# Kernel tuning notes

Measured on AMD Instinct MI355X. Metric: run time of the kernel, lower is better.

The kernel has to match this reference:

```python
import jax, jax.numpy as jnp
import numpy as np

N_NODES = 100000
N_EDGES = 6400000
MIN_DIST = 5.0


def setup_inputs() -> dict:
    key = jax.random.key(0)
    k1, k2, k3 = jax.random.split(key, 3)
    pos = jax.random.normal(k1, (N_NODES, 2), dtype=jnp.float32)
    vel = jax.random.normal(k2, (N_NODES, 2), dtype=jnp.float32)
    edge_index = jax.random.randint(k3, (2, N_EDGES), 0, N_NODES, dtype=jnp.int64)
    return {"pos": pos, "vel": vel, "edge_index": edge_index}


def reference(pos, vel, edge_index):
    # h = [pos, vel] per node, shape [N, 4]
    h = jnp.concatenate([pos, vel], axis=-1)
    src, dst = edge_index[0], edge_index[1]  # PyG: h_j = h[src], h_i = h[dst]
    h_dif = h[src] - h[dst]                  # [E, 4]
    pos_dif = h_dif[:, :2]                   # [E, 2]
    vel_dif = h_dif[:, 2:]                   # [E, 2]

    norm = jnp.linalg.norm(pos_dif, axis=1)  # [E]
    safe_norm = jnp.where(norm > 0, norm, 1.0)
    # coll = -sigmoid(-10*(|d|-min_dist)) * d/|d|, nan_to_num(0) where |d|==0
    coll = jnp.where(
        (norm > 0)[:, None],
        -jax.nn.sigmoid(-10.0 * (norm - MIN_DIST))[:, None] * pos_dif / safe_norm[:, None],
        0.0,
    )                                        # [E, 2]
    mean_in = pos_dif / 30.0 + vel_dif       # [E, 2]

    n = pos.shape[0]
    add_out = jax.ops.segment_sum(coll, dst, num_segments=n)      # scatter add
    sums = jax.ops.segment_sum(mean_in, dst, num_segments=n)
    counts = jax.ops.segment_sum(jnp.ones((dst.shape[0], 1), pos.dtype), dst, num_segments=n)
    mean_out = sums / jnp.maximum(counts, 1.0)                    # scatter mean

    return add_out * 5.0 + mean_out          # [N, 2] acceleration
```

## Files before the change

### kernel.cpp

```cpp
#include <hip/hip_runtime.h>


#define DC      200
#define NBK     512
#define NSEG    512
#define EPB     12500
#define ORDCAP  14400
#define KB      13
#define KBV     16
#define KMAX    15
#define BLOCK   256
#define BBLOCK  1024
#define FBLOCK  1024

__device__ __forceinline__ void edge_math(float4 hs, float4 hd,
                                          float& cx, float& cy, float& mx, float& my) {
    float px = hs.x - hd.x;
    float py = hs.y - hd.y;
    float vx = hs.z - hd.z;
    float vy = hs.w - hd.w;
    float norm = sqrtf(px * px + py * py);
    cx = 0.0f; cy = 0.0f;
    if (norm > 0.0f) {
        float sig = 1.0f / (1.0f + expf(10.0f * (norm - 5.0f)));
        float scale = -sig / norm;
        cx = scale * px;
        cy = scale * py;
    }
    mx = px * (1.0f / 30.0f) + vx;
    my = py * (1.0f / 30.0f) + vy;
}

__global__ __launch_bounds__(BBLOCK) void bin_kernel(
        const int* __restrict__ ei,
        const float2* __restrict__ pos2, const float2* __restrict__ vel2,
        float4* __restrict__ h4, unsigned* __restrict__ binsout,
        int* __restrict__ inclT, int n_edges, int nbb,
        int n_nodes, int hpb) {
    __shared__ __align__(16) unsigned ord[EPB];
    __shared__ int hist[NBK];
    __shared__ int cur[NBK];
    __shared__ int wsum[16];
    __shared__ int wbase[16];

    const int tid  = threadIdx.x;
    const int lane = tid & 63;
    const int wv   = tid >> 6;
    const int bx   = blockIdx.x;
    const long long e0 = (long long)bx * EPB;
    const int n_my = (int)min((long long)EPB, (long long)n_edges - e0);
    if (n_my <= 0) return;

    {
        int i0 = bx * hpb;
        int i1 = min(n_nodes, i0 + hpb);
        for (int i = i0 + tid; i < i1; i += BBLOCK) {
            float2 p = pos2[i];
            float2 v = vel2[i];
            h4[i] = make_float4(p.x, p.y, v.x, v.y);
        }
    }

    const int* __restrict__ srow = ei + e0;
    const int* __restrict__ drow = ei + n_edges + e0;

    for (int i = tid; i < NBK; i += BBLOCK) hist[i] = 0;
    __syncthreads();

    const bool vec = (n_my == EPB) && ((n_edges & 3) == 0) && ((EPB & 3) == 0);
    const int nvec = EPB >> 2;

    int      bq[KBV];
    unsigned wq[KBV];
    #pragma unroll
    for (int q = 0; q < KBV; ++q) bq[q] = -1;

    if (vec) {
        const int4* __restrict__ s4 = reinterpret_cast<const int4*>(srow);
        const int4* __restrict__ d4 = reinterpret_cast<const int4*>(drow);
        #pragma unroll
        for (int q = 0; q < 4; ++q) {
            int v = tid + q * BBLOCK;
            if (v < nvec) {
                int4 ss = s4[v];
                int4 dd = d4[v];
                #pragma unroll
                for (int j = 0; j < 4; ++j) {
                    int d = (&dd.x)[j];
                    int s = (&ss.x)[j];
                    int b = (int)((unsigned)d / DC);
                    bq[q * 4 + j] = b;
                    wq[q * 4 + j] = ((unsigned)s << 8) | (unsigned)(d - b * DC);
                }
            }
        }
    } else {
        #pragma unroll
        for (int q = 0; q < KB; ++q) {
            int idx = tid + q * BBLOCK;
            if (idx < n_my) {
                int d = drow[idx];
                int s = srow[idx];
                int b = (int)((unsigned)d / DC);
                bq[q] = b;
                wq[q] = ((unsigned)s << 8) | (unsigned)(d - b * DC);
            }
        }
    }
    #pragma unroll
    for (int q = 0; q < KBV; ++q)
        if (bq[q] >= 0) atomicAdd(&hist[bq[q]], 1);
    __syncthreads();

    const int nw = NBK >> 6;
    int myinc = 0, myh = 0, myi = 0;
    if (wv < nw) {
        myi = (wv << 6) + lane;
        myh = hist[myi];
        int v = myh;
        #pragma unroll
        for (int m = 1; m < 64; m <<= 1) {
            int u = __shfl_up(v, m);
            if (lane >= m) v += u;
        }
        myinc = v;
        if (lane == 63) wsum[wv] = v;
    }
    __syncthreads();
    if (tid == 0) {
        int run = 0;
        for (int w = 0; w < nw; ++w) { wbase[w] = run; run += wsum[w]; }
    }
    __syncthreads();
    if (wv < nw) {
        int inc = myinc + wbase[wv];
        cur[myi] = inc - myh;
        inclT[(size_t)myi * nbb + bx] = inc;
    }
    __syncthreads();

    #pragma unroll
    for (int q = 0; q < KBV; ++q) {
        if (bq[q] >= 0) {
            int p = atomicAdd(&cur[bq[q]], 1);
            ord[p] = wq[q];
        }
    }
    __syncthreads();

    if (vec) {
        const int4* __restrict__ o4 = reinterpret_cast<const int4*>(ord);
        int4* __restrict__ bo4 = reinterpret_cast<int4*>(binsout + e0);
        for (int i = tid; i < nvec; i += BBLOCK) bo4[i] = o4[i];
    } else {
        unsigned* __restrict__ bo = binsout + e0;
        for (int i = tid; i < n_my; i += BBLOCK) bo[i] = ord[i];
    }
}

__global__ __launch_bounds__(FBLOCK) void fused_kernel(
        const float4* __restrict__ h4, const unsigned* __restrict__ binsout,
        const int* __restrict__ inclT, float* __restrict__ out,
        int nbb, int n_nodes) {
    __shared__ unsigned ord2[ORDCAP];
    __shared__ int spfx[NSEG + 1];
    __shared__ int adj[NSEG];
    __shared__ int hist[DC];
    __shared__ int pfx[DC + 1];
    __shared__ int cur[DC];
    __shared__ int wsum[16];
    __shared__ int wbase[16];

    unsigned short* map = reinterpret_cast<unsigned short*>(ord2);

    const int tid  = threadIdx.x;
    const int lane = tid & 63;
    const int wv   = tid >> 6;
    const int dc   = blockIdx.x;

    for (int j = tid; j < nbb; j += FBLOCK) {
        int hi = inclT[(size_t)dc * nbb + j];
        int lo = (dc > 0) ? inclT[(size_t)(dc - 1) * nbb + j] : 0;
        adj[j] = j * EPB + lo;
        spfx[j + 1] = hi - lo;
    }
    for (int i = tid; i < DC; i += FBLOCK) hist[i] = 0;
    if (tid == 0) spfx[0] = 0;
    __syncthreads();

    const int nw = (nbb + 63) >> 6;
    int myv = 0, myj = -1;
    if (wv < nw) {
        myj = (wv << 6) + lane;
        int v = (myj < nbb) ? spfx[myj + 1] : 0;
        #pragma unroll
        for (int m = 1; m < 64; m <<= 1) {
            int u = __shfl_up(v, m);
            if (lane >= m) v += u;
        }
        myv = v;
        if (lane == 63) wsum[wv] = v;
    }
    __syncthreads();
    if (tid == 0) {
        int run = 0;
        for (int w = 0; w < nw; ++w) { wbase[w] = run; run += wsum[w]; }
    }
    __syncthreads();
    if (wv < nw && myj < nbb) spfx[myj + 1] = myv + wbase[wv];
    __syncthreads();
    int tot = spfx[nbb];
    if (tot > ORDCAP) tot = ORDCAP;
    for (int j = tid; j < nbb; j += FBLOCK) {
        int k0 = spfx[j];
        int k1 = min(spfx[j + 1], ORDCAP);
        adj[j] -= k0;
        for (int k = k0; k < k1; ++k) map[k] = (unsigned short)j;
    }
    __syncthreads();

    unsigned wqr[KMAX];
    #pragma unroll
    for (int q = 0; q < KMAX; ++q) {
        int p = tid + q * FBLOCK;
        if (p < tot) {
            int j = (int)map[p];
            unsigned w = binsout[adj[j] + p];
            wqr[q] = w;
            atomicAdd(&hist[w & 255u], 1);
        }
    }
    __syncthreads();

    const int nwh = (DC + 63) >> 6;
    int mvr = 0, mr = -1, mh = 0;
    if (wv < nwh) {
        mr = (wv << 6) + lane;
        mh = (mr < DC) ? hist[mr] : 0;
        int v = mh;
        #pragma unroll
        for (int m = 1; m < 64; m <<= 1) {
            int u = __shfl_up(v, m);
            if (lane >= m) v += u;
        }
        mvr = v;
        if (lane == 63) wsum[8 + wv] = v;
    }
    __syncthreads();
    if (tid == 0) {
        int run = 0;
        for (int w = 0; w < nwh; ++w) { wbase[8 + w] = run; run += wsum[8 + w]; }
    }
    __syncthreads();
    if (wv < nwh && mr < DC) {
        int inc = mvr + wbase[8 + wv];
        pfx[mr + 1] = inc;
        cur[mr] = inc - mh;
        if (mr == 0) pfx[0] = 0;
    }
    __syncthreads();

    #pragma unroll
    for (int q = 0; q < KMAX; ++q) {
        int p = tid + q * FBLOCK;
        if (p < tot) {
            int pp = atomicAdd(&cur[wqr[q] & 255u], 1);
            ord2[pp] = wqr[q] >> 8;
        }
    }
    __syncthreads();

    const int grp = tid >> 4;
    const int gl  = tid & 15;
    const int base = dc * DC;
    for (int r = grp; r < DC; r += FBLOCK / 16) {
        int n = base + r;
        if (n < n_nodes) {
            int st = pfx[r], en = pfx[r + 1];
            int cnt = en - st;
            float4 hd = h4[n];
            float a0 = 0.f, a1 = 0.f, a2 = 0.f, a3 = 0.f;
            for (int k = st + gl; k < en; k += 16) {
                unsigned s = ord2[k];
                float4 hs = h4[s];
                float cx, cy, mx, my;
                edge_math(hs, hd, cx, cy, mx, my);
                a0 += cx; a1 += cy; a2 += mx; a3 += my;
            }
            #pragma unroll
            for (int m = 8; m >= 1; m >>= 1) {
                a0 += __shfl_xor(a0, m);
                a1 += __shfl_xor(a1, m);
                a2 += __shfl_xor(a2, m);
                a3 += __shfl_xor(a3, m);
            }
            if (gl == 0) {
                float inv = 1.0f / fmaxf((float)cnt, 1.0f);
                float2 o;
                o.x = a0 * 5.0f + a2 * inv;
                o.y = a1 * 5.0f + a3 * inv;
                reinterpret_cast<float2*>(out)[n] = o;
            }
        }
    }
}

__global__ void edge_kernel(const float* __restrict__ pos,
                            const float* __restrict__ vel,
                            const int* __restrict__ ei,
                            float* __restrict__ acc,
                            int n_nodes, int n_edges) {
    int e = blockIdx.x * blockDim.x + threadIdx.x;
    if (e >= n_edges) return;
    int s = ei[e];
    int d = ei[n_edges + e];
    const float2* pos2 = reinterpret_cast<const float2*>(pos);
    const float2* vel2 = reinterpret_cast<const float2*>(vel);
    float4 hs = make_float4(pos2[s].x, pos2[s].y, vel2[s].x, vel2[s].y);
    float4 hd = make_float4(pos2[d].x, pos2[d].y, vel2[d].x, vel2[d].y);
    float cx, cy, mx, my;
    edge_math(hs, hd, cx, cy, mx, my);
    atomicAdd(&acc[0 * n_nodes + d], cx);
    atomicAdd(&acc[1 * n_nodes + d], cy);
    atomicAdd(&acc[2 * n_nodes + d], mx);
    atomicAdd(&acc[3 * n_nodes + d], my);
    atomicAdd(&acc[4 * n_nodes + d], 1.0f);
}

__global__ void finalize_kernel(const float* __restrict__ acc,
                                float* __restrict__ out, int n_nodes) {
    int i = blockIdx.x * blockDim.x + threadIdx.x;
    if (i >= n_nodes) return;
    float cx = acc[0 * n_nodes + i];
    float cy = acc[1 * n_nodes + i];
    float mx = acc[2 * n_nodes + i];
    float my = acc[3 * n_nodes + i];
    float cnt = acc[4 * n_nodes + i];
    float inv = 1.0f / fmaxf(cnt, 1.0f);
    float2 o;
    o.x = cx * 5.0f + mx * inv;
    o.y = cy * 5.0f + my * inv;
    reinterpret_cast<float2*>(out)[i] = o;
}

extern "C" void kernel_launch(void* const* d_in, const int* in_sizes, int n_in,
                              void* d_out, int out_size, void* d_ws, size_t ws_size,
                              hipStream_t stream) {
    const float* pos = (const float*)d_in[0];
    const float* vel = (const float*)d_in[1];
    const int*   ei  = (const int*)d_in[2];
    float* out = (float*)d_out;

    int n_nodes = in_sizes[0] / 2;
    int n_edges = in_sizes[2] / 2;

    int ndc = (n_nodes + DC - 1) / DC;
    int nbb = (int)(((long long)n_edges + EPB - 1) / EPB);
    int hpb = (n_nodes + nbb - 1) / nbb;

    size_t h_off    = 0;
    size_t bo_off   = (h_off + (size_t)n_nodes * 16 + 511) & ~(size_t)511;
    size_t incl_off = (bo_off + (size_t)nbb * EPB * 4 + 511) & ~(size_t)511;
    size_t need     = incl_off + (size_t)NBK * nbb * 4;

    if (ndc <= NBK && nbb <= NSEG && need <= ws_size &&
        (unsigned)n_nodes < (1u << 24)) {
        float4*   h4      = (float4*)((char*)d_ws + h_off);
        unsigned* binsout = (unsigned*)((char*)d_ws + bo_off);
        int*      inclT   = (int*)((char*)d_ws + incl_off);

        bin_kernel<<<nbb, BBLOCK, 0, stream>>>(
            ei, (const float2*)pos, (const float2*)vel, h4,
            binsout, inclT, n_edges, nbb, n_nodes, hpb);

        fused_kernel<<<ndc, FBLOCK, 0, stream>>>(h4, binsout, inclT, out,
                                                 nbb, n_nodes);
    } else {
        float* acc = (float*)d_ws;
        hipMemsetAsync(d_ws, 0, (size_t)5 * n_nodes * sizeof(float), stream);
        int grid_e = (n_edges + BLOCK - 1) / BLOCK;
        edge_kernel<<<grid_e, BLOCK, 0, stream>>>(pos, vel, ei, acc, n_nodes, n_edges);
        int grid_n = (n_nodes + BLOCK - 1) / BLOCK;
        finalize_kernel<<<grid_n, BLOCK, 0, stream>>>(acc, out, n_nodes);
    }
}
```

Measured before the change: 139.8 us.

## Pad per-node edge segments to multiples of four and vectorize gather

Each destination's segment in the shared-memory edge list is padded to a multiple of four. The padding slots are filled with the node's own index, so those edges produce zero difference and contribute nothing. The accumulation loop then reads source indices as uint4 and issues four independent h4 gathers per thread, which raises memory-level parallelism and cuts LDS instructions. Fast-math intrinsics (__expf, __fdividef) replace the exact exp and divides, and there are new clamps against ORDCAP because padding can overflow the shared buffer. If the padded total exceeds capacity, edges could be silently dropped.

```diff
diff --git a/kernel.cpp b/kernel.cpp
--- a/kernel.cpp
+++ b/kernel.cpp
@@ -19,11 +19,12 @@
     float py = hs.y - hd.y;
     float vx = hs.z - hd.z;
     float vy = hs.w - hd.w;
-    float norm = sqrtf(px * px + py * py);
+    float n2 = px * px + py * py;
     cx = 0.0f; cy = 0.0f;
-    if (norm > 0.0f) {
-        float sig = 1.0f / (1.0f + expf(10.0f * (norm - 5.0f)));
-        float scale = -sig / norm;
+    if (n2 > 0.0f) {
+        float norm = sqrtf(n2);
+        float sig = __fdividef(1.0f, 1.0f + __expf(10.0f * (norm - 5.0f)));
+        float scale = -__fdividef(sig, norm);
         cx = scale * px;
         cy = scale * py;
     }
@@ -162,11 +163,11 @@
         const float4* __restrict__ h4, const unsigned* __restrict__ binsout,
         const int* __restrict__ inclT, float* __restrict__ out,
         int nbb, int n_nodes) {
-    __shared__ unsigned ord2[ORDCAP];
+    __shared__ __align__(16) unsigned ord2[ORDCAP];
     __shared__ int spfx[NSEG + 1];
     __shared__ int adj[NSEG];
     __shared__ int hist[DC];
-    __shared__ int pfx[DC + 1];
+    __shared__ int pfx[DC];
     __shared__ int cur[DC];
     __shared__ int wsum[16];
     __shared__ int wbase[16];
@@ -233,11 +234,11 @@
     __syncthreads();
 
     const int nwh = (DC + 63) >> 6;
-    int mvr = 0, mr = -1, mh = 0;
+    int mvr = 0, mr = -1, mph = 0;
     if (wv < nwh) {
         mr = (wv << 6) + lane;
-        mh = (mr < DC) ? hist[mr] : 0;
-        int v = mh;
+        mph = (mr < DC) ? ((hist[mr] + 3) & ~3) : 0;
+        int v = mph;
         #pragma unroll
         for (int m = 1; m < 64; m <<= 1) {
             int u = __shfl_up(v, m);
@@ -253,38 +254,54 @@
     }
     __syncthreads();
     if (wv < nwh && mr < DC) {
-        int inc = mvr + wbase[8 + wv];
-        pfx[mr + 1] = inc;
-        cur[mr] = inc - mh;
-        if (mr == 0) pfx[0] = 0;
-    }
-    __syncthreads();
-
+        int st = min(mvr + wbase[8 + wv] - mph, ORDCAP);
+        pfx[mr] = st;
+        cur[mr] = st;
+    }
+    __syncthreads();
+
+    const int base = dc * DC;
+    for (int r = tid; r < DC; r += FBLOCK) {
+        int h = hist[r];
+        int st = pfx[r];
+        int pe = st + ((h + 3) & ~3);
+        for (int k = st + h; k < pe && k < ORDCAP; ++k)
+            ord2[k] = (unsigned)(base + r);
+    }
     #pragma unroll
     for (int q = 0; q < KMAX; ++q) {
         int p = tid + q * FBLOCK;
         if (p < tot) {
             int pp = atomicAdd(&cur[wqr[q] & 255u], 1);
-            ord2[pp] = wqr[q] >> 8;
+            if (pp < ORDCAP) ord2[pp] = wqr[q] >> 8;
         }
     }
     __syncthreads();
 
     const int grp = tid >> 4;
     const int gl  = tid & 15;
-    const int base = dc * DC;
     for (int r = grp; r < DC; r += FBLOCK / 16) {
         int n = base + r;
         if (n < n_nodes) {
-            int st = pfx[r], en = pfx[r + 1];
-            int cnt = en - st;
+            int st  = pfx[r];
+            int cnt = hist[r];
+            int pe  = min(st + ((cnt + 3) & ~3), ORDCAP & ~3);
             float4 hd = h4[n];
             float a0 = 0.f, a1 = 0.f, a2 = 0.f, a3 = 0.f;
-            for (int k = st + gl; k < en; k += 16) {
-                unsigned s = ord2[k];
-                float4 hs = h4[s];
+            for (int k = st + 4 * gl; k < pe; k += 64) {
+                uint4 s4 = *reinterpret_cast<const uint4*>(&ord2[k]);
+                float4 h0 = h4[s4.x];
+                float4 h1 = h4[s4.y];
+                float4 h2 = h4[s4.z];
+                float4 h3 = h4[s4.w];
                 float cx, cy, mx, my;
-                edge_math(hs, hd, cx, cy, mx, my);
+                edge_math(h0, hd, cx, cy, mx, my);
+                a0 += cx; a1 += cy; a2 += mx; a3 += my;
+                edge_math(h1, hd, cx, cy, mx, my);
+                a0 += cx; a1 += cy; a2 += mx; a3 += my;
+                edge_math(h2, hd, cx, cy, mx, my);
+                a0 += cx; a1 += cy; a2 += mx; a3 += my;
+                edge_math(h3, hd, cx, cy, mx, my);
                 a0 += cx; a1 += cy; a2 += mx; a3 += my;
             }
             #pragma unroll
@@ -295,7 +312,7 @@
                 a3 += __shfl_xor(a3, m);
             }
             if (gl == 0) {
-                float inv = 1.0f / fmaxf((float)cnt, 1.0f);
+                float inv = __fdividef(1.0f, fmaxf((float)cnt, 1.0f));
                 float2 o;
                 o.x = a0 * 5.0f + a2 * inv;
                 o.y = a1 * 5.0f + a3 * inv;
```

Result: no change. 140.9 us (+0.8%).
